# Performance work log

Measured on AMD Instinct MI355X. Metric: run time of the kernel, lower is better.

## Reference

```python
import jax, jax.numpy as jnp
import numpy as np

FEATURE_DIM = 256
ATT_DIM = 128


def setup_inputs() -> dict:
    key = jax.random.key(0)
    k1, k2, k3, k4 = jax.random.split(key, 4)
    x = jax.random.normal(k1, (128, 2048, FEATURE_DIM), dtype=jnp.float32)
    weight = jax.random.normal(k2, (FEATURE_DIM, ATT_DIM), dtype=jnp.float32)
    bias = jax.random.normal(k3, (ATT_DIM,), dtype=jnp.float32)
    context_vec = jax.random.normal(k4, (ATT_DIM, 1), dtype=jnp.float32)
    return {"x": x, "weight": weight, "bias": bias, "context_vec": context_vec}


def reference(x, weight, bias, context_vec):
    # x: [B, T, D]; additive attention scores over T
    eij = jnp.tanh(jnp.einsum("btd,da->bta", x, weight) + bias)  # [B, T, A]
    eij = jnp.einsum("bta,ao->bt", eij, context_vec)             # [B, T]
    # Faithful to original: plain exp (no max subtraction) + eps-stabilized sum
    a = jnp.exp(eij)
    a = a / (jnp.sum(a, axis=1, keepdims=True) + 1e-10)          # [B, T]
    return jnp.einsum("bt,btd->bd", a, x)                        # [B, D]
```

## Files before the change

### kernel.cpp

```cpp
#include <hip/hip_runtime.h>
#include <math.h>

#define BB 128
#define TT 2048
#define DD 256
#define AA 128
#define ROWS (BB*TT)

typedef __attribute__((ext_vector_type(8))) short bf16x8;
typedef __attribute__((ext_vector_type(4))) float f32x4;

__device__ __forceinline__ unsigned short f2bf(float f) {
    unsigned int u = __builtin_bit_cast(unsigned int, f);
    unsigned int r = (u + 0x7FFFu + ((u >> 16) & 1u)) >> 16;
    return (unsigned short)r;
}
__device__ __forceinline__ float bf2f(unsigned short s) {
    unsigned int u = ((unsigned int)s) << 16;
    return __builtin_bit_cast(float, u);
}


__global__ __launch_bounds__(512, 2) void k_mfma(
    const float* __restrict__ x, const float* __restrict__ w,
    const float* __restrict__ bias, const float* __restrict__ ctx,
    float* __restrict__ expv, float* __restrict__ zsum)
{
    __shared__ bf16x8 ldsx[2][1024];
    __shared__ float pred[8][16];

    const int tid  = threadIdx.x;
    const int lane = tid & 63;
    const int wv   = tid >> 6;

    const int colg  = wv * 16 + (lane & 15);
    const int krow0 = (lane >> 4) * 8;
    bf16x8 wh[8], wl[8];
    #pragma unroll
    for (int ks = 0; ks < 8; ++ks) {
        union { bf16x8 v; unsigned short u[8]; } H, L;
        #pragma unroll
        for (int j = 0; j < 8; ++j) {
            float f = w[(ks * 32 + krow0 + j) * AA + colg];
            unsigned short h = f2bf(f);
            H.u[j] = h;
            L.u[j] = f2bf(f - bf2f(h));
        }
        wh[ks] = H.v; wl[ks] = L.v;
    }
    const float bias_l = bias[colg];
    const float ctx_l  = ctx[colg];

    const int srow = tid >> 5;
    const int kg   = tid & 31;
    const int sks  = kg >> 2;
    const int slot = ((kg & 3) << 4) + srow;
    const int wfrag = sks * 64 + (slot ^ sks);

    const int ntiles = 32;
    const int tile0  = blockIdx.x * ntiles;

    float ld[8];
    auto issue_loads = [&](int tile) {
        const float* src = x + (size_t)tile * (16 * DD) + srow * DD + kg * 8;
        float4 a = *(const float4*)(src);
        float4 b = *(const float4*)(src + 4);
        ld[0]=a.x; ld[1]=a.y; ld[2]=a.z; ld[3]=a.w;
        ld[4]=b.x; ld[5]=b.y; ld[6]=b.z; ld[7]=b.w;
    };
    auto write_lds = [&](int buf) {
        union { bf16x8 v; unsigned short u[8]; } H, L;
        #pragma unroll
        for (int j = 0; j < 8; ++j) {
            unsigned short h = f2bf(ld[j]);
            H.u[j] = h;
            L.u[j] = f2bf(ld[j] - bf2f(h));
        }
        ldsx[buf][wfrag]       = H.v;
        ldsx[buf][512 + wfrag] = L.v;
    };

    issue_loads(tile0);
    write_lds(0);
    __syncthreads();

    for (int i = 0; i < ntiles; ++i) {
        const int tile = tile0 + i;
        if (i + 1 < ntiles) issue_loads(tile + 1);

        const int buf = i & 1;
        f32x4 acc = {0.f, 0.f, 0.f, 0.f};
        #pragma unroll
        for (int ks = 0; ks < 8; ++ks) {
            const int rf = ks * 64 + (lane ^ ks);
            bf16x8 ah = ldsx[buf][rf];
            bf16x8 al = ldsx[buf][512 + rf];
            acc = __builtin_amdgcn_mfma_f32_16x16x32_bf16(ah, wh[ks], acc, 0, 0, 0);
            acc = __builtin_amdgcn_mfma_f32_16x16x32_bf16(al, wh[ks], acc, 0, 0, 0);
            acc = __builtin_amdgcn_mfma_f32_16x16x32_bf16(ah, wl[ks], acc, 0, 0, 0);
        }

        #pragma unroll
        for (int r = 0; r < 4; ++r) {
            float v = tanhf(acc[r] + bias_l) * ctx_l;
            v += __shfl_xor(v, 1, 64);
            v += __shfl_xor(v, 2, 64);
            v += __shfl_xor(v, 4, 64);
            v += __shfl_xor(v, 8, 64);
            if ((lane & 15) == 0) pred[wv][(lane >> 4) * 4 + r] = v;
        }
        __syncthreads();

        if (i + 1 < ntiles) write_lds(buf ^ 1);

        if (tid < 16) {
            float s = pred[0][tid] + pred[1][tid] + pred[2][tid] + pred[3][tid]
                    + pred[4][tid] + pred[5][tid] + pred[6][tid] + pred[7][tid];
            float e = expf(s);
            expv[(size_t)tile * 16 + tid] = e;
            float t = e;
            t += __shfl_xor(t, 1, 64);
            t += __shfl_xor(t, 2, 64);
            t += __shfl_xor(t, 4, 64);
            t += __shfl_xor(t, 8, 64);
            if (tid == 0) atomicAdd(&zsum[tile >> 7], t);
        }
        __syncthreads();
    }
}

__global__ __launch_bounds__(256) void k_wsum(
    const float* __restrict__ x, const float* __restrict__ expv,
    const float* __restrict__ zsum, float* __restrict__ pout)
{
    const int b     = blockIdx.x >> 3;
    const int chunk = blockIdx.x & 7;
    const int d     = threadIdx.x;
    const float iz  = 1.f / (zsum[b] + 1e-10f);

    float acc = 0.f;
    const int t0 = chunk * 256;
    #pragma unroll 4
    for (int t = t0; t < t0 + 256; ++t) {
        float wt = expv[b * TT + t] * iz;
        acc = fmaf(wt, x[((size_t)(b * TT + t)) * DD + d], acc);
    }
    pout[((size_t)chunk * BB + b) * DD + d] = acc;
}

__global__ __launch_bounds__(256) void k_final(
    const float* __restrict__ pout, float* __restrict__ out)
{
    const int i = blockIdx.x * 256 + threadIdx.x;
    float s = 0.f;
    #pragma unroll
    for (int c = 0; c < 8; ++c)
        s += pout[(size_t)c * BB * DD + i];
    out[i] = s;
}

extern "C" void kernel_launch(void* const* d_in, const int* in_sizes, int n_in,
                              void* d_out, int out_size, void* d_ws, size_t ws_size,
                              hipStream_t stream)
{
    const float* x    = (const float*)d_in[0];
    const float* w    = (const float*)d_in[1];
    const float* bias = (const float*)d_in[2];
    const float* ctx  = (const float*)d_in[3];
    float* out = (float*)d_out;

    float* ws   = (float*)d_ws;
    float* expv = ws;
    float* zsum = ws + ROWS;
    float* pout = zsum + 256;

    hipMemsetAsync(zsum, 0, 128 * sizeof(float), stream);
    k_mfma <<<512, 512, 0, stream>>>(x, w, bias, ctx, expv, zsum);
    k_wsum <<<BB*8, 256, 0, stream>>>(x, expv, zsum, pout);
    k_final<<<BB*DD/256, 256, 0, stream>>>(pout, out);
}
```

Before: 443.9 us.

## Fuse weighted sum into MFMA scoring kernel to avoid re-reading x

Weighted accumulation of x is moved into the scoring kernel. Each thread keeps the fp32 rows it already loaded in registers and accumulates exp(score)*x, so x is read from global memory once instead of twice. Per-block partial numerators and denominators go to workspace, and a small final kernel combines them and normalizes. This drops the memset, the atomics and a kernel launch. It also halves tiles per block and doubles the requested occupancy, which adds register pressure from the extra buffers and 16KB of reduction LDS.

```diff
diff --git a/kernel.cpp b/kernel.cpp
--- a/kernel.cpp
+++ b/kernel.cpp
@@ -6,6 +6,9 @@
 #define DD 256
 #define AA 128
 #define ROWS (BB*TT)
+#define NTILES 16
+#define NBLK (ROWS/16/NTILES)
+#define BPB 8
 
 typedef __attribute__((ext_vector_type(8))) short bf16x8;
 typedef __attribute__((ext_vector_type(4))) float f32x4;
@@ -21,13 +24,15 @@
 }
 
 
-__global__ __launch_bounds__(512, 2) void k_mfma(
+__global__ __launch_bounds__(512, 4) void k_fused(
     const float* __restrict__ x, const float* __restrict__ w,
     const float* __restrict__ bias, const float* __restrict__ ctx,
-    float* __restrict__ expv, float* __restrict__ zsum)
+    float* __restrict__ pnum, float* __restrict__ pz)
 {
     __shared__ bf16x8 ldsx[2][1024];
     __shared__ float pred[8][16];
+    __shared__ float erow[16];
+    __shared__ float redbuf[16][256];
 
     const int tid  = threadIdx.x;
     const int lane = tid & 63;
@@ -51,24 +56,27 @@
     const float bias_l = bias[colg];
     const float ctx_l  = ctx[colg];
 
-    const int srow = tid >> 5;
-    const int kg   = tid & 31;
-    const int sks  = kg >> 2;
-    const int slot = ((kg & 3) << 4) + srow;
+    const int srow  = tid >> 5;
+    const int kg    = tid & 31;
+    const int sks   = kg >> 2;
+    const int slot  = ((kg & 3) << 4) + srow;
     const int wfrag = sks * 64 + (slot ^ sks);
 
-    const int ntiles = 32;
-    const int tile0  = blockIdx.x * ntiles;
+    const int tile0 = blockIdx.x * NTILES;
 
-    float ld[8];
-    auto issue_loads = [&](int tile) {
+    float ldA[8], ldB[8], nacc[8];
+    #pragma unroll
+    for (int j = 0; j < 8; ++j) nacc[j] = 0.f;
+    float zacc = 0.f;
+
+    auto load_regs = [&](int tile, float (&ld)[8]) {
         const float* src = x + (size_t)tile * (16 * DD) + srow * DD + kg * 8;
         float4 a = *(const float4*)(src);
         float4 b = *(const float4*)(src + 4);
         ld[0]=a.x; ld[1]=a.y; ld[2]=a.z; ld[3]=a.w;
         ld[4]=b.x; ld[5]=b.y; ld[6]=b.z; ld[7]=b.w;
     };
-    auto write_lds = [&](int buf) {
+    auto write_lds = [&](int buf, const float (&ld)[8]) {
         union { bf16x8 v; unsigned short u[8]; } H, L;
         #pragma unroll
         for (int j = 0; j < 8; ++j) {
@@ -80,13 +88,9 @@
         ldsx[buf][512 + wfrag] = L.v;
     };
 
-    issue_loads(tile0);
-    write_lds(0);
-    __syncthreads();
-
-    for (int i = 0; i < ntiles; ++i) {
+    auto step = [&](int i, float (&cur)[8], float (&nxt)[8]) {
         const int tile = tile0 + i;
-        if (i + 1 < ntiles) issue_loads(tile + 1);
+        if (i + 1 < NTILES) load_regs(tile + 1, nxt);
 
         const int buf = i & 1;
         f32x4 acc = {0.f, 0.f, 0.f, 0.f};
@@ -111,52 +115,64 @@
         }
         __syncthreads();
 
-        if (i + 1 < ntiles) write_lds(buf ^ 1);
-
         if (tid < 16) {
             float s = pred[0][tid] + pred[1][tid] + pred[2][tid] + pred[3][tid]
                     + pred[4][tid] + pred[5][tid] + pred[6][tid] + pred[7][tid];
             float e = expf(s);
-            expv[(size_t)tile * 16 + tid] = e;
-            float t = e;
-            t += __shfl_xor(t, 1, 64);
-            t += __shfl_xor(t, 2, 64);
-            t += __shfl_xor(t, 4, 64);
-            t += __shfl_xor(t, 8, 64);
-            if (tid == 0) atomicAdd(&zsum[tile >> 7], t);
+            erow[tid] = e;
+            zacc += e;
         }
+        if (i + 1 < NTILES) write_lds(buf ^ 1, nxt);
         __syncthreads();
+
+        const float ew = erow[srow];
+        #pragma unroll
+        for (int j = 0; j < 8; ++j)
+            nacc[j] = fmaf(ew, cur[j], nacc[j]);
+    };
+
+    load_regs(tile0, ldA);
+    write_lds(0, ldA);
+    __syncthreads();
+
+    for (int i = 0; i < NTILES; i += 2) {
+        step(i,     ldA, ldB);
+        step(i + 1, ldB, ldA);
+    }
+
+    #pragma unroll
+    for (int j = 0; j < 8; ++j)
+        redbuf[srow][kg * 8 + j] = nacc[j];
+    __syncthreads();
+    if (tid < 256) {
+        float s = 0.f;
+        #pragma unroll
+        for (int r = 0; r < 16; ++r) s += redbuf[r][tid];
+        pnum[(size_t)blockIdx.x * 256 + tid] = s;
+    }
+    if (tid < 16) {
+        float z = zacc;
+        z += __shfl_xor(z, 1, 64);
+        z += __shfl_xor(z, 2, 64);
+        z += __shfl_xor(z, 4, 64);
+        z += __shfl_xor(z, 8, 64);
+        if (tid == 0) pz[blockIdx.x] = z;
     }
 }
 
-__global__ __launch_bounds__(256) void k_wsum(
-    const float* __restrict__ x, const float* __restrict__ expv,
-    const float* __restrict__ zsum, float* __restrict__ pout)
+__global__ __launch_bounds__(256) void k_out(
+    const float* __restrict__ pnum, const float* __restrict__ pz,
+    float* __restrict__ out)
 {
-    const int b     = blockIdx.x >> 3;
-    const int chunk = blockIdx.x & 7;
-    const int d     = threadIdx.x;
-    const float iz  = 1.f / (zsum[b] + 1e-10f);
-
-    float acc = 0.f;
-    const int t0 = chunk * 256;
-    #pragma unroll 4
-    for (int t = t0; t < t0 + 256; ++t) {
-        float wt = expv[b * TT + t] * iz;
-        acc = fmaf(wt, x[((size_t)(b * TT + t)) * DD + d], acc);
+    const int b = blockIdx.x;
+    const int d = threadIdx.x;
+    float s = 0.f, z = 0.f;
+    #pragma unroll
+    for (int c = 0; c < BPB; ++c) {
+        s += pnum[((size_t)(b * BPB + c)) * 256 + d];
+        z += pz[b * BPB + c];
     }
-    pout[((size_t)chunk * BB + b) * DD + d] = acc;
-}
-
-__global__ __launch_bounds__(256) void k_final(
-    const float* __restrict__ pout, float* __restrict__ out)
-{
-    const int i = blockIdx.x * 256 + threadIdx.x;
-    float s = 0.f;
-    #pragma unroll
-    for (int c = 0; c < 8; ++c)
-        s += pout[(size_t)c * BB * DD + i];
-    out[i] = s;
+    out[b * DD + d] = s / (z + 1e-10f);
 }
 
 extern "C" void kernel_launch(void* const* d_in, const int* in_sizes, int n_in,
@@ -170,12 +186,9 @@
     float* out = (float*)d_out;
 
     float* ws   = (float*)d_ws;
-    float* expv = ws;
-    float* zsum = ws + ROWS;
-    float* pout = zsum + 256;
+    float* pnum = ws;
+    float* pz   = ws + (size_t)NBLK * 256;
 
-    hipMemsetAsync(zsum, 0, 128 * sizeof(float), stream);
-    k_mfma <<<512, 512, 0, stream>>>(x, w, bias, ctx, expv, zsum);
-    k_wsum <<<BB*8, 256, 0, stream>>>(x, expv, zsum, pout);
-    k_final<<<BB*DD/256, 256, 0, stream>>>(pout, out);
+    k_fused<<<NBLK, 512, 0, stream>>>(x, w, bias, ctx, pnum, pz);
+    k_out  <<<BB,   256, 0, stream>>>(pnum, pz, out);
 }
```

Result: slower. 469.6 us (+5.8%).
